# Optimization experiments

Hardware: AMD Instinct MI355X
Metric: run time of the kernel (lower is better)

The kernel has to match this reference:

```python
import jax, jax.numpy as jnp
import numpy as np

EMBEDS = 512
HEADS = 4
HEAD_SIZE = 512  # head_size = embeds in Block.__init__
D_HEAD = EMBEDS // HEADS  # 128
LN_EPS = 512.0  # nn.LayerNorm(embeds, head_size) -> eps=head_size (faithful to source bug)
B, T = 4096, 4  # T must equal heads=4 for the mask broadcast in the source to work


def layer_norm(x, g, b, eps=LN_EPS):
    mu = jnp.mean(x, axis=-1, keepdims=True)
    var = jnp.mean(jnp.square(x - mu), axis=-1, keepdims=True)
    return (x - mu) / jnp.sqrt(var + eps) * g + b


def setup_inputs() -> dict:
    key = jax.random.key(0)
    ks = jax.random.split(key, 12)
    s_qkv = 1.0 / np.sqrt(D_HEAD)
    s_proj = 1.0 / np.sqrt(HEAD_SIZE)
    s_ff1 = 1.0 / np.sqrt(EMBEDS)
    s_ff2 = 1.0 / np.sqrt(4 * EMBEDS)
    return {
        "x": jax.random.normal(ks[0], (B, T, EMBEDS), dtype=jnp.float32),
        "Wq": jax.random.uniform(ks[1], (D_HEAD, HEAD_SIZE), jnp.float32, -s_qkv, s_qkv),
        "Wk": jax.random.uniform(ks[2], (D_HEAD, HEAD_SIZE), jnp.float32, -s_qkv, s_qkv),
        "Wv": jax.random.uniform(ks[3], (D_HEAD, HEAD_SIZE), jnp.float32, -s_qkv, s_qkv),
        "Wp": jax.random.uniform(ks[4], (HEAD_SIZE, EMBEDS), jnp.float32, -s_proj, s_proj),
        "bp": jax.random.uniform(ks[5], (EMBEDS,), jnp.float32, -s_proj, s_proj),
        "W1": jax.random.uniform(ks[6], (EMBEDS, 4 * EMBEDS), jnp.float32, -s_ff1, s_ff1),
        "b1": jax.random.uniform(ks[7], (4 * EMBEDS,), jnp.float32, -s_ff1, s_ff1),
        "W2": jax.random.uniform(ks[8], (4 * EMBEDS, EMBEDS), jnp.float32, -s_ff2, s_ff2),
        "b2": jax.random.uniform(ks[9], (EMBEDS,), jnp.float32, -s_ff2, s_ff2),
        "ln1_g": jnp.ones((EMBEDS,), jnp.float32),
        "ln1_b": jnp.zeros((EMBEDS,), jnp.float32),
        "ln2_g": jnp.ones((EMBEDS,), jnp.float32),
        "ln2_b": jnp.zeros((EMBEDS,), jnp.float32),
    }


def reference(x, Wq, Wk, Wv, Wp, bp, W1, b1, W2, b2, ln1_g, ln1_b, ln2_g, ln2_b):
    Bx, Tx, C = x.shape
    xh = x.reshape(Bx, Tx, HEADS, C // HEADS)          # [B,T,4,128]
    q = jnp.einsum('bthc,cd->bthd', xh, Wq)            # [B,T,4,512]
    k = jnp.einsum('bthc,cd->bthd', xh, Wk)
    v = jnp.einsum('bthc,cd->bthd', xh, Wv)
    # scores over the HEAD axis (faithful to source): [B,T,4,4]
    wei = jnp.einsum('btid,btjd->btij', q, k) * (HEAD_SIZE ** -0.5)
    causal = jnp.tril(jnp.ones((Tx, Tx), dtype=bool))  # broadcast over trailing [4,4]; requires T==4
    wei = jnp.where(causal, wei, -jnp.inf)
    wei = jax.nn.softmax(wei, axis=-1)                 # dropout omitted (eval mode)
    att = jnp.einsum('btij,btjd->btid', wei, v)        # [B,T,4,512]
    y = jnp.einsum('btid,de->btie', att, Wp) + bp      # [B,T,4,512]
    # residual broadcast: x [B,T,512] + y [B,T,4,512] -> [B,T,4,512]
    x1 = layer_norm(x[:, :, None, :] + y, ln1_g, ln1_b)
    h = jax.nn.gelu(jnp.einsum('btie,ef->btif', x1, W1) + b1, approximate=False)
    h = jnp.einsum('btif,fe->btie', h, W2) + b2
    return layer_norm(x1 + h, ln2_g, ln2_b)            # [B,T,4,512]
```

## Files before the change

kernel.cpp:

```cpp
#include <hip/hip_runtime.h>
#include <hip/hip_bf16.h>
#include <math.h>

typedef __bf16 bf16x8 __attribute__((ext_vector_type(8)));
typedef float f32x4 __attribute__((ext_vector_type(4)));
typedef unsigned short u16;
typedef unsigned int u32;
typedef u16 u16x4 __attribute__((ext_vector_type(4)));
typedef u16 u16x8 __attribute__((ext_vector_type(8)));

#define TOKENS 16384
#define MROWS  65536

__device__ __forceinline__ u16 f2bf(float f) {
  union { __hip_bfloat16 h; u16 u; } c;
  c.h = __float2bfloat16(f);
  return c.u;
}
__device__ __forceinline__ float bf2f(u16 u) {
  union { u16 u; __hip_bfloat16 h; } c;
  c.u = u;
  return __bfloat162float(c.h);
}
__device__ __forceinline__ float gelu_f(float u) {
  float y2 = u * fmaf(0.07135481283f, u * u, 1.595769122f);
  float e = __expf(-y2);
  return u / (1.f + e);
}
__device__ __forceinline__ void gload16(const void* g, void* l) {
  __builtin_amdgcn_global_load_lds(
      (const __attribute__((address_space(1))) void*)g,
      (__attribute__((address_space(3))) void*)l, 16, 0, 0);
}

__global__ void kprep_G(const float* __restrict__ Wq, const float* __restrict__ Wk,
                        u16* __restrict__ Gbf) {
  int id = blockIdx.x * 256 + threadIdx.x;
  int c = id >> 7, c2 = id & 127;
  const float4* a = (const float4*)(Wq + (size_t)c * 512);
  const float4* b = (const float4*)(Wk + (size_t)c2 * 512);
  float s = 0.f;
#pragma unroll 8
  for (int i = 0; i < 128; ++i) {
    float4 xa = a[i], yb = b[i];
    s += xa.x * yb.x + xa.y * yb.y + xa.z * yb.z + xa.w * yb.w;
  }
  Gbf[id] = f2bf(s * 0.044194173824159216f);
}

__global__ void kprep_Wvp(const float* __restrict__ Wv, const float* __restrict__ Wp,
                          u16* __restrict__ WvpT) {
  int id = blockIdx.x * 256 + threadIdx.x;
  int e = id >> 7, c = id & 127;
  float s = 0.f;
#pragma unroll 4
  for (int d = 0; d < 512; ++d) s += Wv[(size_t)c * 512 + d] * Wp[(size_t)d * 512 + e];
  WvpT[id] = f2bf(s);
}

__global__ __launch_bounds__(256) void kprep_W1T(const float* __restrict__ W1,
                                                 u16* __restrict__ W1T) {
  __shared__ u16 Lt[64][72];
  int tid = threadIdx.x;
  int bf = blockIdx.x, be = blockIdx.y;
#pragma unroll
  for (int rnd = 0; rnd < 4; ++rnd) {
    int r = rnd * 16 + (tid >> 4);
    int f4 = (tid & 15) * 4;
    float4 v = *(const float4*)(W1 + (size_t)(be * 64 + r) * 2048 + bf * 64 + f4);
    Lt[r][f4] = f2bf(v.x); Lt[r][f4 + 1] = f2bf(v.y);
    Lt[r][f4 + 2] = f2bf(v.z); Lt[r][f4 + 3] = f2bf(v.w);
  }
  __syncthreads();
  int fl = tid >> 2, eg = (tid & 3) * 16;
  u16x8 o0, o1;
#pragma unroll
  for (int q = 0; q < 8; ++q) { o0[q] = Lt[eg + q][fl]; o1[q] = Lt[eg + 8 + q][fl]; }
  u16* dst = W1T + (size_t)(bf * 64 + fl) * 512 + be * 64 + eg;
  *(u16x8*)dst = o0;
  *(u16x8*)(dst + 8) = o1;
}

__global__ __launch_bounds__(256) void kprep_W2T(const float* __restrict__ W2,
                                                 u16* __restrict__ W2T) {
  __shared__ u16 Lt[64][72];
  int tid = threadIdx.x;
  int bf = blockIdx.x, be = blockIdx.y;
#pragma unroll
  for (int rnd = 0; rnd < 4; ++rnd) {
    int r = rnd * 16 + (tid >> 4);
    int e4 = (tid & 15) * 4;
    float4 v = *(const float4*)(W2 + (size_t)(bf * 64 + r) * 512 + be * 64 + e4);
    Lt[r][e4] = f2bf(v.x); Lt[r][e4 + 1] = f2bf(v.y);
    Lt[r][e4 + 2] = f2bf(v.z); Lt[r][e4 + 3] = f2bf(v.w);
  }
  __syncthreads();
  int aa = bf & 1, fb = bf >> 1;
  int el = tid >> 2, g = tid & 3;
  u16x8 o0, o1;
#pragma unroll
  for (int q = 0; q < 8; ++q) {
    int fs0 = g * 16 + q, fs1 = g * 16 + 8 + q;
    o0[q] = Lt[(fs0 & 3) * 16 + ((fs0 >> 2) & 15)][el];
    o1[q] = Lt[(fs1 & 3) * 16 + ((fs1 >> 2) & 15)][el];
  }
  u16* dst = W2T + (size_t)(be * 64 + el) * 2048 + fb * 128 + aa * 64 + g * 16;
  *(u16x8*)dst = o0;
  *(u16x8*)(dst + 8) = o1;
}

__global__ __launch_bounds__(256) void ktoken(const float* __restrict__ x,
                                              const u16* __restrict__ Gbf,
                                              u16* __restrict__ Z) {
  __shared__ float Ss[4 * 512];
  __shared__ __align__(16) u16 Gs[16384];
  int tid = threadIdx.x;
  int wave = tid >> 6, lane = tid & 63;
  int tok = blockIdx.x * 4 + wave;
  char* GsC = (char*)Gs;
#pragma unroll
  for (int it = 0; it < 8; ++it)
    gload16(Gbf + (size_t)(it * 256 + tid) * 8, GsC + it * 4096 + wave * 1024);
  {
    const float4* xs = (const float4*)(x + (size_t)tok * 512);
    float4* sw = (float4*)(Ss + wave * 512);
    sw[lane] = xs[lane];
    sw[64 + lane] = xs[64 + lane];
  }
  __syncthreads();

  const float* Sw = Ss + wave * 512;
  const u32* Grow = (const u32*)Gs;
  float a[4][2] = {{0.f, 0.f}, {0.f, 0.f}, {0.f, 0.f}, {0.f, 0.f}};
#pragma unroll 4
  for (int c = 0; c < 128; ++c) {
    u32 g2 = Grow[c * 64 + lane];
    float glo = __uint_as_float(g2 << 16);
    float ghi = __uint_as_float(g2 & 0xFFFF0000u);
    float s0 = Sw[c], s1 = Sw[128 + c], s2 = Sw[256 + c], s3 = Sw[384 + c];
    a[0][0] += s0 * glo; a[0][1] += s0 * ghi;
    a[1][0] += s1 * glo; a[1][1] += s1 * ghi;
    a[2][0] += s2 * glo; a[2][1] += s2 * ghi;
    a[3][0] += s3 * glo; a[3][1] += s3 * ghi;
  }
  float w[16];
#pragma unroll
  for (int j = 0; j < 4; ++j) {
    float sj0 = Sw[j * 128 + 2 * lane];
    float sj1 = Sw[j * 128 + 2 * lane + 1];
#pragma unroll
    for (int i = 0; i < 4; ++i)
      w[i * 4 + j] = a[i][0] * sj0 + a[i][1] * sj1;
  }
#pragma unroll
  for (int off = 1; off < 64; off <<= 1)
#pragma unroll
    for (int k = 0; k < 16; ++k) w[k] += __shfl_xor(w[k], off);
  float p[4][4];
#pragma unroll
  for (int i = 0; i < 4; ++i) {
    float m = w[i * 4];
    for (int j = 1; j <= i; ++j) m = fmaxf(m, w[i * 4 + j]);
    float s = 0.f;
    for (int j = 0; j <= i; ++j) { p[i][j] = __expf(w[i * 4 + j] - m); s += p[i][j]; }
    float inv = 1.f / s;
    for (int j = 0; j <= i; ++j) p[i][j] *= inv;
    for (int j = i + 1; j < 4; ++j) p[i][j] = 0.f;
  }
  int c = lane * 2;
  u32* zout = (u32*)(Z + (size_t)tok * 512);
#pragma unroll
  for (int i = 0; i < 4; ++i) {
    float z0 = 0.f, z1 = 0.f;
#pragma unroll
    for (int j = 0; j < 4; ++j) {
      z0 += p[i][j] * Sw[j * 128 + c];
      z1 += p[i][j] * Sw[j * 128 + c + 1];
    }
    zout[i * 64 + lane] = (u32)f2bf(z0) | ((u32)f2bf(z1) << 16);
  }
}

__global__ __launch_bounds__(512) void kattn(const u16* __restrict__ Z,
                                             const u16* __restrict__ WvpT,
                                             const float* __restrict__ bp,
                                             const float* __restrict__ x,
                                             const float* __restrict__ g1,
                                             const float* __restrict__ bln1,
                                             u16* __restrict__ X1) {
  __shared__ __align__(16) u16 AO[32768];
  __shared__ float rsum[64 * 4];
  __shared__ float rsq[64 * 4];
  __shared__ float mus[64];
  __shared__ float rss[64];
  char* smem = (char*)AO;
  int tid = threadIdx.x;
  int lane = tid & 63, wid = tid >> 6;
  int wm = wid >> 2, wnq = wid & 3;
  int lane_lo = lane & 15, lane_hi = lane >> 4;
  int m0 = blockIdx.x * 64;
  {
    const u16* Zs = Z + (size_t)m0 * 128;
#pragma unroll
    for (int it = 0; it < 2; ++it) {
      int idx8 = it * 512 + tid;
      int row = idx8 >> 4, u = idx8 & 15;
      gload16(Zs + (size_t)row * 128 + ((u ^ (row & 7)) << 3), smem + idx8 * 16);
    }
    const float* xsrc = x + (size_t)(m0 >> 2) * 512;
#pragma unroll
    for (int it = 0; it < 4; ++it) {
      int idx = it * 512 + tid;
      gload16(xsrc + idx * 4, smem + 16384 + idx * 16);
    }
  }
  __syncthreads();
  f32x4 acc[2][8];
#pragma unroll
  for (int mi = 0; mi < 2; ++mi)
#pragma unroll
    for (int ni = 0; ni < 8; ++ni) acc[mi][ni] = (f32x4){0.f, 0.f, 0.f, 0.f};
#pragma unroll
  for (int ks = 0; ks < 4; ++ks) {
    bf16x8 af[2];
#pragma unroll
    for (int mi = 0; mi < 2; ++mi) {
      int row = wm * 32 + mi * 16 + lane_lo;
      int byte = (row * 256 + (ks * 32 + lane_hi * 8) * 2) ^ ((row & 7) << 4);
      af[mi] = *(const bf16x8*)(smem + byte);
    }
#pragma unroll
    for (int ni = 0; ni < 8; ++ni) {
      int n = wnq * 128 + ni * 16 + lane_lo;
      bf16x8 bfr = *(const bf16x8*)(WvpT + (size_t)n * 128 + ks * 32 + lane_hi * 8);
#pragma unroll
      for (int mi = 0; mi < 2; ++mi)
        acc[mi][ni] = __builtin_amdgcn_mfma_f32_16x16x32_bf16(af[mi], bfr, acc[mi][ni], 0, 0, 0);
    }
  }
  float bpv[8], g1v[8], blv[8];
#pragma unroll
  for (int ni = 0; ni < 8; ++ni) {
    int col = wnq * 128 + ni * 16 + lane_lo;
    bpv[ni] = bp[col]; g1v[ni] = g1[col]; blv[ni] = bln1[col];
  }
  const float* xs = (const float*)(smem + 16384);
#pragma unroll
  for (int mi = 0; mi < 2; ++mi) {
#pragma unroll
    for (int j = 0; j < 4; ++j) {
      int rl = wm * 32 + mi * 16 + lane_hi * 4 + j;
      int tl = wm * 8 + mi * 4 + lane_hi;
      float s = 0.f, q = 0.f;
#pragma unroll
      for (int ni = 0; ni < 8; ++ni) {
        int col = wnq * 128 + ni * 16 + lane_lo;
        float val = acc[mi][ni][j] + bpv[ni] + xs[tl * 512 + col];
        acc[mi][ni][j] = val;
        s += val; q += val * val;
      }
#pragma unroll
      for (int off = 1; off < 16; off <<= 1) { s += __shfl_xor(s, off); q += __shfl_xor(q, off); }
      if (lane_lo == 0) { rsum[rl * 4 + wnq] = s; rsq[rl * 4 + wnq] = q; }
    }
  }
  __syncthreads();
  if (tid < 64) {
    float s = rsum[tid * 4] + rsum[tid * 4 + 1] + rsum[tid * 4 + 2] + rsum[tid * 4 + 3];
    float q = rsq[tid * 4] + rsq[tid * 4 + 1] + rsq[tid * 4 + 2] + rsq[tid * 4 + 3];
    float mu = s * (1.f / 512.f);
    float var = q * (1.f / 512.f) - mu * mu;
    mus[tid] = mu;
    rss[tid] = rsqrtf(var + 512.0f);
  }
  __syncthreads();
#pragma unroll
  for (int mi = 0; mi < 2; ++mi) {
#pragma unroll
    for (int j = 0; j < 4; ++j) {
      int rl = wm * 32 + mi * 16 + lane_hi * 4 + j;
      float mu = mus[rl], rs = rss[rl];
#pragma unroll
      for (int ni = 0; ni < 8; ++ni) {
        int col = wnq * 128 + ni * 16 + lane_lo;
        AO[rl * 512 + col] = f2bf((acc[mi][ni][j] - mu) * rs * g1v[ni] + blv[ni]);
      }
    }
  }
  __syncthreads();
  {
    bf16x8* dst = (bf16x8*)(X1 + (size_t)m0 * 512);
    const bf16x8* s8 = (const bf16x8*)AO;
#pragma unroll
    for (int it = 0; it < 8; ++it) dst[it * 512 + tid] = s8[it * 512 + tid];
  }
}

template<int KDIM>
__device__ __forceinline__ void gemm256(const u16* __restrict__ Ap,
                                        const u16* __restrict__ Bp,
                                        u16* Ab, u16* Bb,
                                        int wid, int lane, f32x4 acc[4][4]) {
  char* AbC = (char*)Ab;
  char* BbC = (char*)Bb;
  const int lane_lo = lane & 15, lane_hi = lane >> 4;
  const int wm = wid >> 1, wn = wid & 1;
  const int rl8 = lane >> 3, u8 = lane & 7;
  for (int k0 = 0; k0 < KDIM; k0 += 64) {
#pragma unroll
    for (int i = 0; i < 4; ++i) {
      int row = wid * 32 + i * 8 + rl8;
      int usw = u8 ^ (row & 7);
      gload16(Ap + (size_t)row * KDIM + k0 + usw * 8, AbC + wid * 4096 + i * 1024);
    }
#pragma unroll
    for (int i = 0; i < 2; ++i) {
      int row = wid * 16 + i * 8 + rl8;
      int usw = u8 ^ (row & 7);
      gload16(Bp + (size_t)row * KDIM + k0 + usw * 8, BbC + wid * 2048 + i * 1024);
    }
    __syncthreads();
#pragma unroll
    for (int ks = 0; ks < 2; ++ks) {
      bf16x8 av[4], bv[4];
#pragma unroll
      for (int mi = 0; mi < 4; ++mi) {
        int row = wm * 64 + mi * 16 + lane_lo;
        int usw = (ks * 4 + lane_hi) ^ (row & 7);
        av[mi] = *(const bf16x8*)(AbC + row * 128 + usw * 16);
      }
#pragma unroll
      for (int ni = 0; ni < 4; ++ni) {
        int row = wn * 64 + ni * 16 + lane_lo;
        int usw = (ks * 4 + lane_hi) ^ (row & 7);
        bv[ni] = *(const bf16x8*)(BbC + row * 128 + usw * 16);
      }
#pragma unroll
      for (int mi = 0; mi < 4; ++mi)
#pragma unroll
        for (int ni = 0; ni < 4; ++ni)
          acc[mi][ni] = __builtin_amdgcn_mfma_f32_16x16x32_bf16(av[mi], bv[ni], acc[mi][ni], 0, 0, 0);
    }
    __syncthreads();
  }
}

template<int KDIM>
__device__ __forceinline__ void gemm_core_db(const u16* __restrict__ Ap,
                                             const u16* __restrict__ Bp,
                                             u16* AbBase, u16* BbBase,
                                             int wid, int lane, f32x4 acc[4][4]) {
  const int lane_lo = lane & 15, lane_hi = lane >> 4;
  const int wm = wid >> 1, wn = wid & 1;
  const int rl8 = lane >> 3, u8 = lane & 7;

  auto stage = [&](int buf, int k0) {
    char* AbC = (char*)AbBase + buf * 16384;
    char* BbC = (char*)BbBase + buf * 16384;
#pragma unroll
    for (int i = 0; i < 4; ++i) {
      int row = wid * 32 + i * 8 + rl8;
      int usw = u8 ^ (row & 7);
      size_t goff = (size_t)row * KDIM + k0 + usw * 8;
      gload16(Ap + goff, AbC + wid * 4096 + i * 1024);
      gload16(Bp + goff, BbC + wid * 4096 + i * 1024);
    }
  };
  auto compute = [&](int buf) {
    char* AbC = (char*)AbBase + buf * 16384;
    char* BbC = (char*)BbBase + buf * 16384;
#pragma unroll
    for (int ks = 0; ks < 2; ++ks) {
      bf16x8 av[4], bv[4];
#pragma unroll
      for (int mi = 0; mi < 4; ++mi) {
        int row = wm * 64 + mi * 16 + lane_lo;
        int usw = (ks * 4 + lane_hi) ^ (row & 7);
        av[mi] = *(const bf16x8*)(AbC + row * 128 + usw * 16);
      }
#pragma unroll
      for (int ni = 0; ni < 4; ++ni) {
        int row = wn * 64 + ni * 16 + lane_lo;
        int usw = (ks * 4 + lane_hi) ^ (row & 7);
        bv[ni] = *(const bf16x8*)(BbC + row * 128 + usw * 16);
      }
#pragma unroll
      for (int mi = 0; mi < 4; ++mi)
#pragma unroll
        for (int ni = 0; ni < 4; ++ni)
          acc[mi][ni] = __builtin_amdgcn_mfma_f32_16x16x32_bf16(av[mi], bv[ni], acc[mi][ni], 0, 0, 0);
    }
  };

  stage(0, 0);
  asm volatile("s_waitcnt vmcnt(0)" ::: "memory");
  __builtin_amdgcn_s_barrier();
  __builtin_amdgcn_sched_barrier(0);
  int cur = 0;
  for (int k0 = 64; k0 < KDIM; k0 += 64) {
    stage(cur ^ 1, k0);
    compute(cur);
    asm volatile("s_waitcnt vmcnt(0)" ::: "memory");
    __builtin_amdgcn_s_barrier();
    __builtin_amdgcn_sched_barrier(0);
    cur ^= 1;
  }
  compute(cur);
}

__global__ __launch_bounds__(512) void kff1(const u16* __restrict__ X1s,
                                            const u16* __restrict__ W1T,
                                            const float* __restrict__ b1v,
                                            u16* __restrict__ H) {
  __shared__ __align__(16) u16 Ab[16384];
  __shared__ __align__(16) u16 Bb[8192];
  int tid = threadIdx.x, lane = tid & 63, wid = tid >> 6;
  int lane_lo = lane & 15, lane_hi = lane >> 4;
  int wm = wid >> 1, wn = wid & 1;
  int nwg = gridDim.x, bid = blockIdx.x;
  int m256 = nwg >> 4;
  int xcd = bid & 7, idx = bid >> 3;
  int mb = xcd * (m256 >> 3) + (idx >> 4);
  int nb = idx & 15;
  const u16* Ap = X1s + (size_t)mb * 256 * 512;
  const u16* Bp = W1T + (size_t)nb * 128 * 512;
  f32x4 acc[4][4];
#pragma unroll
  for (int mi = 0; mi < 4; ++mi)
#pragma unroll
    for (int ni = 0; ni < 4; ++ni) acc[mi][ni] = (f32x4){0.f, 0.f, 0.f, 0.f};
  gemm256<512>(Ap, Bp, Ab, Bb, wid, lane, acc);
  float bvals[4];
#pragma unroll
  for (int ni = 0; ni < 4; ++ni) bvals[ni] = b1v[nb * 128 + wn * 64 + ni * 16 + lane_lo];
  int colb = nb * 128 + (wn * 16 + lane_lo) * 4;
#pragma unroll
  for (int mi = 0; mi < 4; ++mi)
#pragma unroll
    for (int j = 0; j < 4; ++j) {
      int rl = wm * 64 + mi * 16 + lane_hi * 4 + j;
      u16x4 pk;
#pragma unroll
      for (int ni = 0; ni < 4; ++ni)
        pk[ni] = f2bf(gelu_f(acc[mi][ni][j] + bvals[ni]));
      *(u16x4*)(H + ((size_t)mb * 256 + rl) * 2048 + colb) = pk;
    }
}

__global__ __launch_bounds__(256) void kff2(const u16* __restrict__ H,
                                            const u16* __restrict__ W2T,
                                            const float* __restrict__ b2v,
                                            u16* __restrict__ X1y) {
  __shared__ __align__(16) u16 Ab[16384];
  __shared__ __align__(16) u16 Bb[16384];
  int tid = threadIdx.x, lane = tid & 63, wid = tid >> 6;
  int nwg = gridDim.x, bid = blockIdx.x;
  int m128 = nwg >> 2;
  int xcd = bid & 7, idx = bid >> 3;
  int mb = xcd * (m128 >> 3) + (idx >> 2);
  int nb = idx & 3;
  const u16* Ap = H + (size_t)mb * 128 * 2048;
  const u16* Bp = W2T + (size_t)nb * 128 * 2048;
  f32x4 acc[4][4];
#pragma unroll
  for (int mi = 0; mi < 4; ++mi)
#pragma unroll
    for (int ni = 0; ni < 4; ++ni) acc[mi][ni] = (f32x4){0.f, 0.f, 0.f, 0.f};
  gemm_core_db<2048>(Ap, Bp, Ab, Bb, wid, lane, acc);
  int lane_lo = lane & 15, lane_hi = lane >> 4;
  int wm = wid >> 1, wn = wid & 1;
#pragma unroll
  for (int mi = 0; mi < 4; ++mi)
#pragma unroll
    for (int j = 0; j < 4; ++j) {
      int rl = wm * 64 + mi * 16 + lane_hi * 4 + j;
      size_t row = (size_t)mb * 128 + rl;
      u16* xrow = X1y + row * 512 + nb * 128;
#pragma unroll
      for (int ni = 0; ni < 4; ++ni) {
        int col = wn * 64 + ni * 16 + lane_lo;
        float val = acc[mi][ni][j] + b2v[nb * 128 + col] + bf2f(xrow[col]);
        xrow[col] = f2bf(val);
      }
    }
}

__global__ __launch_bounds__(512) void kln2(const u16* __restrict__ Y,
                                            const float* __restrict__ g2,
                                            const float* __restrict__ bb2,
                                            float* __restrict__ out) {
  int wid = threadIdx.x >> 6, lane = threadIdx.x & 63;
  size_t row = (size_t)blockIdx.x * 8 + wid;
  u16x8 v = *(const u16x8*)(Y + row * 512 + lane * 8);
  float f[8];
  float s = 0.f, q = 0.f;
#pragma unroll
  for (int k = 0; k < 8; ++k) {
    f[k] = bf2f(v[k]);
    s += f[k]; q += f[k] * f[k];
  }
#pragma unroll
  for (int off = 1; off < 64; off <<= 1) { s += __shfl_xor(s, off); q += __shfl_xor(q, off); }
  float mu = s * (1.f / 512.f);
  float rs = rsqrtf(q * (1.f / 512.f) - mu * mu + 512.0f);
  float4 ga = *(const float4*)(g2 + lane * 8);
  float4 gb = *(const float4*)(g2 + lane * 8 + 4);
  float4 ba = *(const float4*)(bb2 + lane * 8);
  float4 bb = *(const float4*)(bb2 + lane * 8 + 4);
  float4 o0, o1;
  o0.x = (f[0] - mu) * rs * ga.x + ba.x;
  o0.y = (f[1] - mu) * rs * ga.y + ba.y;
  o0.z = (f[2] - mu) * rs * ga.z + ba.z;
  o0.w = (f[3] - mu) * rs * ga.w + ba.w;
  o1.x = (f[4] - mu) * rs * gb.x + bb.x;
  o1.y = (f[5] - mu) * rs * gb.y + bb.y;
  o1.z = (f[6] - mu) * rs * gb.z + bb.z;
  o1.w = (f[7] - mu) * rs * gb.w + bb.w;
  float* orow = out + row * 512 + lane * 8;
  *(float4*)orow = o0;
  *(float4*)(orow + 4) = o1;
}

extern "C" void kernel_launch(void* const* d_in, const int* in_sizes, int n_in,
                              void* d_out, int out_size, void* d_ws, size_t ws_size,
                              hipStream_t stream) {
  const float* x   = (const float*)d_in[0];
  const float* Wq  = (const float*)d_in[1];
  const float* Wk  = (const float*)d_in[2];
  const float* Wv  = (const float*)d_in[3];
  const float* Wp  = (const float*)d_in[4];
  const float* bp  = (const float*)d_in[5];
  const float* W1  = (const float*)d_in[6];
  const float* b1  = (const float*)d_in[7];
  const float* W2  = (const float*)d_in[8];
  const float* b2  = (const float*)d_in[9];
  const float* g1  = (const float*)d_in[10];
  const float* bb1 = (const float*)d_in[11];
  const float* g2  = (const float*)d_in[12];
  const float* bb2 = (const float*)d_in[13];
  float* out = (float*)d_out;

  char* ws = (char*)d_ws;
  u16* Gbf  = (u16*)ws;
  u16* WvpT = (u16*)(ws + (256 << 10));
  u16* W1T  = (u16*)(ws + (1 << 20));
  u16* W2T  = (u16*)(ws + (3 << 20));
  u16* Z    = (u16*)(ws + (5 << 20));
  u16* X1   = (u16*)(ws + (21 << 20));
  u16* H    = (u16*)(ws + (85ull << 20));

  hipLaunchKernelGGL(kprep_G,   dim3(64),        dim3(256), 0, stream, Wq, Wk, Gbf);
  hipLaunchKernelGGL(kprep_Wvp, dim3(256),       dim3(256), 0, stream, Wv, Wp, WvpT);
  hipLaunchKernelGGL(kprep_W1T, dim3(32, 8),     dim3(256), 0, stream, W1, W1T);
  hipLaunchKernelGGL(kprep_W2T, dim3(32, 8),     dim3(256), 0, stream, W2, W2T);
  hipLaunchKernelGGL(ktoken,    dim3(4096),      dim3(256), 0, stream, x, Gbf, Z);
  hipLaunchKernelGGL(kattn,     dim3(1024),      dim3(512), 0, stream, Z, WvpT, bp, x, g1, bb1, X1);

  const size_t hbase = 85ull << 20;
  int S = 64;
  for (int c = 2; c <= 64; c <<= 1) {
    if (hbase + (268435456ull / (size_t)c) <= ws_size) { S = c; break; }
  }
  int Ms = MROWS / S;
  for (int s = 0; s < S; ++s) {
    const u16* x1s = X1 + (size_t)s * Ms * 512;
    hipLaunchKernelGGL(kff1, dim3((Ms / 256) * 16), dim3(512), 0, stream, x1s, W1T, b1, H);
    hipLaunchKernelGGL(kff2, dim3((Ms / 128) * 4),  dim3(256), 0, stream, H, W2T, b2,
                       X1 + (size_t)s * Ms * 512);
  }
  hipLaunchKernelGGL(kln2, dim3(8192), dim3(512), 0, stream, X1, g2, bb2, out);
}
```

Measured before the change: 578.1 us.

## Fuse token attention-mixing kernel into Wvp projection and LayerNorm kernel

Merges the per-token score/softmax kernel (ktoken) with the attention-projection + LN1 kernel (kattn), so the mixed activations Z are written to swizzled shared memory instead of round-tripping through global memory. Each 512-thread block now loads G and the 16 tokens of x once and computes the softmax mixing for its own 64 rows before the MFMA projection. This removes one launch and the Z write/read traffic. In exchange, shared memory grows to about 80KB per block, which may lower occupancy, and the scalar scoring phase now runs inside the MFMA kernel with fewer G reloads amortized per token.

```diff
diff --git a/kernel.cpp b/kernel.cpp
--- a/kernel.cpp
+++ b/kernel.cpp
@@ -109,112 +109,87 @@
   *(u16x8*)(dst + 8) = o1;
 }
 
-__global__ __launch_bounds__(256) void ktoken(const float* __restrict__ x,
+__global__ __launch_bounds__(512) void kfused(const float* __restrict__ x,
                                               const u16* __restrict__ Gbf,
-                                              u16* __restrict__ Z) {
-  __shared__ float Ss[4 * 512];
-  __shared__ __align__(16) u16 Gs[16384];
-  int tid = threadIdx.x;
-  int wave = tid >> 6, lane = tid & 63;
-  int tok = blockIdx.x * 4 + wave;
-  char* GsC = (char*)Gs;
-#pragma unroll
-  for (int it = 0; it < 8; ++it)
-    gload16(Gbf + (size_t)(it * 256 + tid) * 8, GsC + it * 4096 + wave * 1024);
-  {
-    const float4* xs = (const float4*)(x + (size_t)tok * 512);
-    float4* sw = (float4*)(Ss + wave * 512);
-    sw[lane] = xs[lane];
-    sw[64 + lane] = xs[64 + lane];
-  }
-  __syncthreads();
-
-  const float* Sw = Ss + wave * 512;
-  const u32* Grow = (const u32*)Gs;
-  float a[4][2] = {{0.f, 0.f}, {0.f, 0.f}, {0.f, 0.f}, {0.f, 0.f}};
-#pragma unroll 4
-  for (int c = 0; c < 128; ++c) {
-    u32 g2 = Grow[c * 64 + lane];
-    float glo = __uint_as_float(g2 << 16);
-    float ghi = __uint_as_float(g2 & 0xFFFF0000u);
-    float s0 = Sw[c], s1 = Sw[128 + c], s2 = Sw[256 + c], s3 = Sw[384 + c];
-    a[0][0] += s0 * glo; a[0][1] += s0 * ghi;
-    a[1][0] += s1 * glo; a[1][1] += s1 * ghi;
-    a[2][0] += s2 * glo; a[2][1] += s2 * ghi;
-    a[3][0] += s3 * glo; a[3][1] += s3 * ghi;
-  }
-  float w[16];
-#pragma unroll
-  for (int j = 0; j < 4; ++j) {
-    float sj0 = Sw[j * 128 + 2 * lane];
-    float sj1 = Sw[j * 128 + 2 * lane + 1];
-#pragma unroll
-    for (int i = 0; i < 4; ++i)
-      w[i * 4 + j] = a[i][0] * sj0 + a[i][1] * sj1;
-  }
-#pragma unroll
-  for (int off = 1; off < 64; off <<= 1)
-#pragma unroll
-    for (int k = 0; k < 16; ++k) w[k] += __shfl_xor(w[k], off);
-  float p[4][4];
-#pragma unroll
-  for (int i = 0; i < 4; ++i) {
-    float m = w[i * 4];
-    for (int j = 1; j <= i; ++j) m = fmaxf(m, w[i * 4 + j]);
-    float s = 0.f;
-    for (int j = 0; j <= i; ++j) { p[i][j] = __expf(w[i * 4 + j] - m); s += p[i][j]; }
-    float inv = 1.f / s;
-    for (int j = 0; j <= i; ++j) p[i][j] *= inv;
-    for (int j = i + 1; j < 4; ++j) p[i][j] = 0.f;
-  }
-  int c = lane * 2;
-  u32* zout = (u32*)(Z + (size_t)tok * 512);
-#pragma unroll
-  for (int i = 0; i < 4; ++i) {
-    float z0 = 0.f, z1 = 0.f;
-#pragma unroll
-    for (int j = 0; j < 4; ++j) {
-      z0 += p[i][j] * Sw[j * 128 + c];
-      z1 += p[i][j] * Sw[j * 128 + c + 1];
-    }
-    zout[i * 64 + lane] = (u32)f2bf(z0) | ((u32)f2bf(z1) << 16);
-  }
-}
-
-__global__ __launch_bounds__(512) void kattn(const u16* __restrict__ Z,
-                                             const u16* __restrict__ WvpT,
-                                             const float* __restrict__ bp,
-                                             const float* __restrict__ x,
-                                             const float* __restrict__ g1,
-                                             const float* __restrict__ bln1,
-                                             u16* __restrict__ X1) {
-  __shared__ __align__(16) u16 AO[32768];
-  __shared__ float rsum[64 * 4];
-  __shared__ float rsq[64 * 4];
-  __shared__ float mus[64];
-  __shared__ float rss[64];
-  char* smem = (char*)AO;
+                                              const u16* __restrict__ WvpT,
+                                              const float* __restrict__ bp,
+                                              const float* __restrict__ g1,
+                                              const float* __restrict__ bln1,
+                                              u16* __restrict__ X1) {
+  __shared__ __align__(16) char smem[81920];
   int tid = threadIdx.x;
   int lane = tid & 63, wid = tid >> 6;
+  int m0 = blockIdx.x * 64;
+  int tok0 = blockIdx.x * 16;
+#pragma unroll
+  for (int it = 0; it < 4; ++it)
+    gload16(Gbf + (size_t)(it * 512 + tid) * 8, smem + (it * 512 + tid) * 16);
+  {
+    const float* xsrc = x + (size_t)tok0 * 512;
+#pragma unroll
+    for (int it = 0; it < 4; ++it)
+      gload16(xsrc + (it * 512 + tid) * 4, smem + 32768 + (it * 512 + tid) * 16);
+  }
+  __syncthreads();
+  float* Xs = (float*)(smem + 32768);
+  const u32* Grow = (const u32*)smem;
+  char* Zbase = smem + 65536;
+  for (int tt = 0; tt < 2; ++tt) {
+    int tl = wid * 2 + tt;
+    const float* Sw = Xs + tl * 512;
+    float a[4][2] = {{0.f, 0.f}, {0.f, 0.f}, {0.f, 0.f}, {0.f, 0.f}};
+#pragma unroll 4
+    for (int c = 0; c < 128; ++c) {
+      u32 g2 = Grow[c * 64 + lane];
+      float glo = __uint_as_float(g2 << 16);
+      float ghi = __uint_as_float(g2 & 0xFFFF0000u);
+      float s0 = Sw[c], s1 = Sw[128 + c], s2 = Sw[256 + c], s3 = Sw[384 + c];
+      a[0][0] += s0 * glo; a[0][1] += s0 * ghi;
+      a[1][0] += s1 * glo; a[1][1] += s1 * ghi;
+      a[2][0] += s2 * glo; a[2][1] += s2 * ghi;
+      a[3][0] += s3 * glo; a[3][1] += s3 * ghi;
+    }
+    float w[16];
+#pragma unroll
+    for (int j = 0; j < 4; ++j) {
+      float sj0 = Sw[j * 128 + 2 * lane];
+      float sj1 = Sw[j * 128 + 2 * lane + 1];
+#pragma unroll
+      for (int i = 0; i < 4; ++i)
+        w[i * 4 + j] = a[i][0] * sj0 + a[i][1] * sj1;
+    }
+#pragma unroll
+    for (int off = 1; off < 64; off <<= 1)
+#pragma unroll
+      for (int k = 0; k < 16; ++k) w[k] += __shfl_xor(w[k], off);
+    float p[4][4];
+#pragma unroll
+    for (int i = 0; i < 4; ++i) {
+      float m = w[i * 4];
+      for (int j = 1; j <= i; ++j) m = fmaxf(m, w[i * 4 + j]);
+      float s = 0.f;
+      for (int j = 0; j <= i; ++j) { p[i][j] = __expf(w[i * 4 + j] - m); s += p[i][j]; }
+      float inv = 1.f / s;
+      for (int j = 0; j <= i; ++j) p[i][j] *= inv;
+      for (int j = i + 1; j < 4; ++j) p[i][j] = 0.f;
+    }
+    int c2 = lane * 2;
+#pragma unroll
+    for (int i = 0; i < 4; ++i) {
+      float z0 = 0.f, z1 = 0.f;
+#pragma unroll
+      for (int j = 0; j < 4; ++j) {
+        z0 += p[i][j] * Sw[j * 128 + c2];
+        z1 += p[i][j] * Sw[j * 128 + c2 + 1];
+      }
+      int row = tl * 4 + i;
+      int byte = (row * 256 + lane * 4) ^ ((row & 7) << 4);
+      *(u32*)(Zbase + byte) = (u32)f2bf(z0) | ((u32)f2bf(z1) << 16);
+    }
+  }
+  __syncthreads();
   int wm = wid >> 2, wnq = wid & 3;
   int lane_lo = lane & 15, lane_hi = lane >> 4;
-  int m0 = blockIdx.x * 64;
-  {
-    const u16* Zs = Z + (size_t)m0 * 128;
-#pragma unroll
-    for (int it = 0; it < 2; ++it) {
-      int idx8 = it * 512 + tid;
-      int row = idx8 >> 4, u = idx8 & 15;
-      gload16(Zs + (size_t)row * 128 + ((u ^ (row & 7)) << 3), smem + idx8 * 16);
-    }
-    const float* xsrc = x + (size_t)(m0 >> 2) * 512;
-#pragma unroll
-    for (int it = 0; it < 4; ++it) {
-      int idx = it * 512 + tid;
-      gload16(xsrc + idx * 4, smem + 16384 + idx * 16);
-    }
-  }
-  __syncthreads();
   f32x4 acc[2][8];
 #pragma unroll
   for (int mi = 0; mi < 2; ++mi)
@@ -227,7 +202,7 @@
     for (int mi = 0; mi < 2; ++mi) {
       int row = wm * 32 + mi * 16 + lane_lo;
       int byte = (row * 256 + (ks * 32 + lane_hi * 8) * 2) ^ ((row & 7) << 4);
-      af[mi] = *(const bf16x8*)(smem + byte);
+      af[mi] = *(const bf16x8*)(Zbase + byte);
     }
 #pragma unroll
     for (int ni = 0; ni < 8; ++ni) {
@@ -238,13 +213,17 @@
         acc[mi][ni] = __builtin_amdgcn_mfma_f32_16x16x32_bf16(af[mi], bfr, acc[mi][ni], 0, 0, 0);
     }
   }
+  __syncthreads();
+  float* rsum = (float*)Zbase;
+  float* rsq  = (float*)(Zbase + 4096);
+  float* mus  = (float*)(Zbase + 8192);
+  float* rss  = (float*)(Zbase + 8448);
   float bpv[8], g1v[8], blv[8];
 #pragma unroll
   for (int ni = 0; ni < 8; ++ni) {
     int col = wnq * 128 + ni * 16 + lane_lo;
     bpv[ni] = bp[col]; g1v[ni] = g1[col]; blv[ni] = bln1[col];
   }
-  const float* xs = (const float*)(smem + 16384);
 #pragma unroll
   for (int mi = 0; mi < 2; ++mi) {
 #pragma unroll
@@ -255,7 +234,7 @@
 #pragma unroll
       for (int ni = 0; ni < 8; ++ni) {
         int col = wnq * 128 + ni * 16 + lane_lo;
-        float val = acc[mi][ni][j] + bpv[ni] + xs[tl * 512 + col];
+        float val = acc[mi][ni][j] + bpv[ni] + Xs[tl * 512 + col];
         acc[mi][ni][j] = val;
         s += val; q += val * val;
       }
@@ -274,6 +253,7 @@
     rss[tid] = rsqrtf(var + 512.0f);
   }
   __syncthreads();
+  u16* AO = (u16*)smem;
 #pragma unroll
   for (int mi = 0; mi < 2; ++mi) {
 #pragma unroll
@@ -545,7 +525,6 @@
   u16* WvpT = (u16*)(ws + (256 << 10));
   u16* W1T  = (u16*)(ws + (1 << 20));
   u16* W2T  = (u16*)(ws + (3 << 20));
-  u16* Z    = (u16*)(ws + (5 << 20));
   u16* X1   = (u16*)(ws + (21 << 20));
   u16* H    = (u16*)(ws + (85ull << 20));
 
@@ -553,8 +532,8 @@
   hipLaunchKernelGGL(kprep_Wvp, dim3(256),       dim3(256), 0, stream, Wv, Wp, WvpT);
   hipLaunchKernelGGL(kprep_W1T, dim3(32, 8),     dim3(256), 0, stream, W1, W1T);
   hipLaunchKernelGGL(kprep_W2T, dim3(32, 8),     dim3(256), 0, stream, W2, W2T);
-  hipLaunchKernelGGL(ktoken,    dim3(4096),      dim3(256), 0, stream, x, Gbf, Z);
-  hipLaunchKernelGGL(kattn,     dim3(1024),      dim3(512), 0, stream, Z, WvpT, bp, x, g1, bb1, X1);
+  hipLaunchKernelGGL(kfused,    dim3(1024),      dim3(512), 0, stream, x, Gbf, WvpT,
+                     bp, g1, bb1, X1);
 
   const size_t hbase = 85ull << 20;
   int S = 64;
```

Result: faster. 562.2 us (-2.7%).
